# Performance work log

Hardware: AMD Instinct MI355X
Metric: run time of the kernel (lower is better)

## Reference

```python
import jax, jax.numpy as jnp
import numpy as np

B, HW, C = 32, 56, 128
WS, SS, NH = 7, 3, 4
HD = C // NH
SCALE = HD ** -0.5
NWIN = (HW // WS) ** 2  # 64 windows per image
N = WS * WS             # 49 tokens per window


def _build_constants():
    # relative position index [N, N] into flattened (13*13) bias table
    coords = np.stack(np.meshgrid(np.arange(WS), np.arange(WS), indexing='ij'))  # [2,7,7]
    cf = coords.reshape(2, -1)                       # [2,49]
    rel = cf[:, :, None] - cf[:, None, :]            # [2,49,49]
    rel = rel.transpose(1, 2, 0).copy()              # [49,49,2]
    rel[:, :, 0] += WS - 1
    rel[:, :, 1] += WS - 1
    rel[:, :, 0] *= 2 * WS - 1
    pos_index = rel.sum(-1)                          # [49,49]
    # shifted-window attention mask [nW, N, N]
    img = np.zeros((HW, HW))
    sl = (slice(0, -WS), slice(-WS, -SS), slice(-SS, None))
    cnt = 0
    for h in sl:
        for w in sl:
            img[h, w] = cnt
            cnt += 1
    mw = img.reshape(HW // WS, WS, HW // WS, WS).transpose(0, 2, 1, 3).reshape(NWIN, N)
    am = mw[:, None, :] - mw[:, :, None]             # unsqueeze(1) - unsqueeze(2)
    am = np.where(am != 0, -100.0, 0.0).astype(np.float32)
    return jnp.asarray(pos_index), jnp.asarray(am)

POS_INDEX, ATTN_MASK = _build_constants()


def _ln(x, w, b, eps=1e-5):
    mu = x.mean(-1, keepdims=True)
    var = ((x - mu) ** 2).mean(-1, keepdims=True)
    return (x - mu) * jax.lax.rsqrt(var + eps) * w + b


def setup_inputs() -> dict:
    key = jax.random.key(0)
    ks = jax.random.split(key, 10)
    s = 0.02
    return {
        'x': jax.random.normal(ks[0], (B, HW * HW, C), jnp.float32),
        'norm1_w': jnp.ones((C,), jnp.float32),
        'norm1_b': jnp.zeros((C,), jnp.float32),
        'qkv_w': jax.random.normal(ks[1], (C, 3 * C), jnp.float32) * s,
        'qkv_b': jax.random.normal(ks[2], (3 * C,), jnp.float32) * s,
        'proj_w': jax.random.normal(ks[3], (C, C), jnp.float32) * s,
        'proj_b': jax.random.normal(ks[4], (C,), jnp.float32) * s,
        'pos_bias_table': jax.random.normal(ks[5], (2 * WS - 1, 2 * WS - 1, NH), jnp.float32) * s,
        'mlp_w1': jax.random.normal(ks[6], (C, 4 * C), jnp.float32) * s,
        'mlp_b1': jnp.zeros((4 * C,), jnp.float32),
        'mlp_w2': jax.random.normal(ks[7], (4 * C, C), jnp.float32) * s,
        'mlp_b2': jnp.zeros((C,), jnp.float32),
        'norm2_w': jnp.ones((C,), jnp.float32),
        'norm2_b': jnp.zeros((C,), jnp.float32),
    }


def reference(x, norm1_w, norm1_b, qkv_w, qkv_b, proj_w, proj_b, pos_bias_table,
              mlp_w1, mlp_b1, mlp_w2, mlp_b2, norm2_w, norm2_b):
    G = HW // WS  # grid of windows per side
    Bw = B * NWIN
    shortcut = x
    y = _ln(x, norm1_w, norm1_b).reshape(B, HW, HW, C)
    # cyclic shift
    y = jnp.roll(y, (-SS, -SS), axis=(1, 2))
    # window partition -> [B*nW, 49, C]
    yw = y.reshape(B, G, WS, G, WS, C).transpose(0, 1, 3, 2, 4, 5).reshape(Bw, N, C)
    # qkv projection
    qkv = (yw @ qkv_w + qkv_b).reshape(Bw, N, 3, NH, HD).transpose(2, 0, 3, 1, 4)
    q, k, v = qkv[0] * SCALE, qkv[1], qkv[2]  # [Bw, NH, N, HD]
    attn = jnp.einsum('bhnd,bhmd->bhnm', q, k)
    # relative position bias [NH, N, N]
    bias = pos_bias_table.reshape(-1, NH)[POS_INDEX]  # [N,N,NH]
    attn = attn + bias.transpose(2, 0, 1)[None]
    # shift mask per window
    attn = attn.reshape(B, NWIN, NH, N, N) + ATTN_MASK[None, :, None]
    attn = jax.nn.softmax(attn.reshape(Bw, NH, N, N), axis=-1)
    out = jnp.einsum('bhnm,bhmd->bhnd', attn, v).transpose(0, 2, 1, 3).reshape(Bw, N, C)
    out = out @ proj_w + proj_b
    # window reverse
    out = out.reshape(B, G, G, WS, WS, C).transpose(0, 1, 3, 2, 4, 5).reshape(B, HW, HW, C)
    out = jnp.roll(out, (SS, SS), axis=(1, 2)).reshape(B, HW * HW, C)
    x = shortcut + out
    h = _ln(x, norm2_w, norm2_b)
    h = jax.nn.gelu(h @ mlp_w1 + mlp_b1, approximate=False) @ mlp_w2 + mlp_b2
    return x + h
```

## Files before the change

kernel.cpp:

```cpp
#include <hip/hip_runtime.h>
#include <hip/hip_bf16.h>

#define NTOK 100352
#define SCALE_Q 0.17677669529663687f

typedef __bf16 bf16x8 __attribute__((ext_vector_type(8)));
typedef float f32x4 __attribute__((ext_vector_type(4)));
struct bf2 { __hip_bfloat16 x, y; };
struct __align__(8) bh4 { __hip_bfloat16 a, b, c, d; };

__device__ __forceinline__ int wt_to_tok(int wt) {
  int w = wt / 49, n = wt - w * 49;
  int b = w >> 6, wi = w & 63;
  int gh = wi >> 3, gw = wi & 7;
  int r = n / 7, c = n - r * 7;
  int hs = gh * 7 + r + 3; if (hs >= 56) hs -= 56;
  int ws = gw * 7 + c + 3; if (ws >= 56) ws -= 56;
  return (b * 56 + hs) * 56 + ws;
}

__device__ __forceinline__ float gelu_sig(float v) {
  return v / (1.0f + __expf(-1.702f * v));
}

__global__ __launch_bounds__(256) void prep_all(const float* __restrict__ qkvw,
                                                const float* __restrict__ projw,
                                                const float* __restrict__ w1,
                                                const float* __restrict__ w2,
                                                __hip_bfloat16* __restrict__ dst) {
  int i = blockIdx.x * 256 + threadIdx.x;
  float v;
  if (i < 49152) { int n = i >> 7, k = i & 127; v = qkvw[k * 384 + n]; }
  else if (i < 65536) { int j = i - 49152; int n = j >> 7, k = j & 127; v = projw[k * 128 + n]; }
  else if (i < 131072) { int j = i - 65536; int n = j >> 7, k = j & 127; v = w1[k * 512 + n]; }
  else { int j = i - 131072; int n = j / 512, k = j - n * 512; v = w2[k * 128 + n]; }
  dst[i] = __float2bfloat16(v);
}

__global__ __launch_bounds__(256) void ln1_apply(const float* __restrict__ x,
                                                 const float* __restrict__ nw,
                                                 const float* __restrict__ nb,
                                                 __hip_bfloat16* __restrict__ xn) {
  int wt = blockIdx.x * 4 + (threadIdx.x >> 6);
  int lane = threadIdx.x & 63;
  int tok = wt_to_tok(wt);
  float2 v = *(const float2*)(x + (size_t)tok * 128 + lane * 2);
  float s = v.x + v.y, ss = v.x * v.x + v.y * v.y;
#pragma unroll
  for (int off = 32; off; off >>= 1) {
    s += __shfl_xor(s, off);
    ss += __shfl_xor(ss, off);
  }
  float mu = s * (1.0f / 128.0f);
  float rstd = rsqrtf(ss * (1.0f / 128.0f) - mu * mu + 1e-5f);
  float2 wv = *(const float2*)(nw + lane * 2);
  float2 bv = *(const float2*)(nb + lane * 2);
  bf2 o;
  o.x = __float2bfloat16((v.x - mu) * rstd * wv.x + bv.x);
  o.y = __float2bfloat16((v.y - mu) * rstd * wv.y + bv.y);
  *(bf2*)(xn + (size_t)wt * 128 + lane * 2) = o;
}

__global__ __launch_bounds__(256) void attn_mfma(const __hip_bfloat16* __restrict__ qkv,
                                                 const float* __restrict__ ptab,
                                                 __hip_bfloat16* __restrict__ attnout) {
  __shared__ __align__(16) char lds[4 * 12288];
  const int tid = threadIdx.x;
  const int lane = tid & 63, h = tid >> 6;
  const int w = blockIdx.x;
  const int wi = w & 63, gh = wi >> 3, gw = wi & 7;
  char* Pl = lds + h * 12288;
  char* VTl = Pl + 8192;
  const int lxi = lane & 15, lq = lane >> 4, lg4 = (lane >> 4) * 4;

  const __hip_bfloat16* base = qkv + (size_t)w * 49 * 384 + h * 32;
  __hip_bfloat16* op = attnout + (size_t)w * 49 * 128 + h * 32;

  bf16x8 qa[4], kb[4];
#pragma unroll
  for (int mi = 0; mi < 4; ++mi) {
    int t = mi * 16 + lxi; if (t > 48) t = 48;
    qa[mi] = *(const bf16x8*)(base + (size_t)t * 384 + lq * 8);
    kb[mi] = *(const bf16x8*)(base + (size_t)t * 384 + 128 + lq * 8);
  }
  {
    union { bf16x8 v; __hip_bfloat16 e[8]; } vv[4];
    const __hip_bfloat16* vp = base + (size_t)(lane < 49 ? lane : 0) * 384 + 256;
#pragma unroll
    for (int q = 0; q < 4; ++q) vv[q].v = *(const bf16x8*)(vp + q * 8);
    __hip_bfloat16 z = __float2bfloat16(0.0f);
#pragma unroll
    for (int q = 0; q < 4; ++q)
#pragma unroll
      for (int e = 0; e < 8; ++e) {
        int d = q * 8 + e;
        __hip_bfloat16 val = (lane < 49) ? vv[q].e[e] : z;
        *(__hip_bfloat16*)(VTl + d * 128 + ((lane * 2) ^ ((d & 7) << 4))) = val;
      }
  }

  f32x4 s[4][4] = {};
#pragma unroll
  for (int mi = 0; mi < 4; ++mi)
#pragma unroll
    for (int ni = 0; ni < 4; ++ni)
      s[mi][ni] = __builtin_amdgcn_mfma_f32_16x16x32_bf16(qa[mi], kb[ni], s[mi][ni], 0, 0, 0);

  int rj[4], cj[4], cntj[4], jbad[4];
#pragma unroll
  for (int ni = 0; ni < 4; ++ni) {
    int jc = ni * 16 + lxi;
    jbad[ni] = (jc > 48);
    int jj = jbad[ni] ? 48 : jc;
    rj[ni] = jj / 7; cj[ni] = jj - rj[ni] * 7;
    int hj = gh * 7 + rj[ni], wj = gw * 7 + cj[ni];
    cntj[ni] = (hj < 49 ? 0 : (hj < 53 ? 3 : 6)) + (wj < 49 ? 0 : (wj < 53 ? 1 : 2));
  }
#pragma unroll
  for (int mi = 0; mi < 4; ++mi)
#pragma unroll
    for (int j = 0; j < 4; ++j) {
      int i = mi * 16 + lg4 + j; if (i > 48) i = 48;
      int ri = i / 7, ci = i - ri * 7;
      int hi_ = gh * 7 + ri, wi_ = gw * 7 + ci;
      int cnti = (hi_ < 49 ? 0 : (hi_ < 53 ? 3 : 6)) + (wi_ < 49 ? 0 : (wi_ < 53 ? 1 : 2));
#pragma unroll
      for (int ni = 0; ni < 4; ++ni) {
        float b = ptab[((ri - rj[ni] + 6) * 13 + (ci - cj[ni] + 6)) * 4 + h];
        float val = s[mi][ni][j] * SCALE_Q + b;
        if (cnti != cntj[ni]) val -= 100.0f;
        if (jbad[ni]) val = -1e30f;
        s[mi][ni][j] = val;
      }
    }

#pragma unroll
  for (int mi = 0; mi < 4; ++mi)
#pragma unroll
    for (int j = 0; j < 4; ++j) {
      float m = fmaxf(fmaxf(s[mi][0][j], s[mi][1][j]), fmaxf(s[mi][2][j], s[mi][3][j]));
#pragma unroll
      for (int off = 8; off; off >>= 1) m = fmaxf(m, __shfl_xor(m, off));
      float e[4], sum = 0.0f;
#pragma unroll
      for (int ni = 0; ni < 4; ++ni) { e[ni] = __expf(s[mi][ni][j] - m); sum += e[ni]; }
#pragma unroll
      for (int off = 8; off; off >>= 1) sum += __shfl_xor(sum, off);
      float inv = 1.0f / sum;
#pragma unroll
      for (int ni = 0; ni < 4; ++ni) s[mi][ni][j] = e[ni] * inv;
    }

#pragma unroll
  for (int mi = 0; mi < 4; ++mi)
#pragma unroll
    for (int j = 0; j < 4; ++j) {
      int row = mi * 16 + lg4 + j;
      int sw = (row & 7) << 4;
      char* prow = Pl + row * 128;
#pragma unroll
      for (int ni = 0; ni < 4; ++ni)
        *(__hip_bfloat16*)(prow + (((ni * 16 + lxi) * 2) ^ sw)) =
            __float2bfloat16(s[mi][ni][j]);
    }

  __syncthreads();

  f32x4 o[4][2] = {};
#pragma unroll
  for (int ks = 0; ks < 2; ++ks) {
    bf16x8 pa[4], vb[2];
#pragma unroll
    for (int mi = 0; mi < 4; ++mi) {
      int row = mi * 16 + lxi;
      pa[mi] = *(const bf16x8*)(Pl + row * 128 + ((ks * 64 + lq * 16) ^ ((row & 7) << 4)));
    }
#pragma unroll
    for (int ni = 0; ni < 2; ++ni) {
      int row = ni * 16 + lxi;
      vb[ni] = *(const bf16x8*)(VTl + row * 128 + ((ks * 64 + lq * 16) ^ ((row & 7) << 4)));
    }
#pragma unroll
    for (int mi = 0; mi < 4; ++mi)
#pragma unroll
      for (int ni = 0; ni < 2; ++ni)
        o[mi][ni] = __builtin_amdgcn_mfma_f32_16x16x32_bf16(pa[mi], vb[ni], o[mi][ni], 0, 0, 0);
  }

#pragma unroll
  for (int mi = 0; mi < 4; ++mi)
#pragma unroll
    for (int j = 0; j < 4; ++j) {
      int q = mi * 16 + lg4 + j;
      if (q < 49) {
#pragma unroll
        for (int ni = 0; ni < 2; ++ni)
          op[(size_t)q * 128 + ni * 16 + lxi] = __float2bfloat16(o[mi][ni][j]);
      }
    }
}

template<int EPI>
__global__ __launch_bounds__(256) void gemm_mfma(
    const __hip_bfloat16* __restrict__ A, int lda, int NB,
    const __hip_bfloat16* __restrict__ Wt,
    const float* __restrict__ bias,
    void* __restrict__ outv, int ldo,
    __hip_bfloat16* __restrict__ out2,
    const float* __restrict__ nw, const float* __restrict__ nb,
    const float* __restrict__ resf, int K)
{
  __shared__ __align__(16) char AsB[128 * 256];
  __shared__ float redS[256], redQ[256];
  const int bid = blockIdx.x;
  const int xcd = bid & 7, tt = bid >> 3;
  const int nbk = tt % NB, mseq = tt / NB;
  const int m0 = (mseq * 8 + xcd) * 128, n0 = nbk * 128;
  const int tid = threadIdx.x;
  const int srow = tid >> 1;
  const int scol = (tid & 1) * 64;
  const int lane = tid & 63, wid = tid >> 6;
  const int wm = wid >> 1, wn = wid & 1;
  const int lrow = lane & 15, lq = lane >> 4;

  f32x4 acc[4][4] = {};

  for (int k0 = 0; k0 < K; k0 += 128) {
    {
      const char* ap = (const char*)A + ((size_t)(m0 + srow) * lda + k0 + scol) * 2;
      char* dst = AsB + srow * 256;
      int sw = (srow & 7) << 4;
#pragma unroll
      for (int t = 0; t < 8; ++t) {
        int4 raw = *(const int4*)(ap + t * 16);
        *(int4*)(dst + ((scol * 2 + t * 16) ^ sw)) = raw;
      }
    }
    __syncthreads();
#pragma unroll
    for (int ks = 0; ks < 4; ++ks) {
      int kb = ks * 64 + lq * 16;
      bf16x8 af[4], bfr[4];
#pragma unroll
      for (int mi = 0; mi < 4; ++mi) {
        int r = wm * 64 + mi * 16 + lrow;
        af[mi] = *(const bf16x8*)(AsB + r * 256 + (kb ^ ((r & 7) << 4)));
      }
#pragma unroll
      for (int ni = 0; ni < 4; ++ni) {
        int n = n0 + wn * 64 + ni * 16 + lrow;
        bfr[ni] = *(const bf16x8*)(Wt + (size_t)n * K + k0 + ks * 32 + lq * 8);
      }
#pragma unroll
      for (int mi = 0; mi < 4; ++mi)
#pragma unroll
        for (int ni = 0; ni < 4; ++ni)
          acc[mi][ni] = __builtin_amdgcn_mfma_f32_16x16x32_bf16(af[mi], bfr[ni], acc[mi][ni], 0, 0, 0);
    }
    __syncthreads();
  }

  float bv[4];
#pragma unroll
  for (int ni = 0; ni < 4; ++ni) bv[ni] = bias[n0 + wn * 64 + ni * 16 + lrow];

  if (EPI == 4) {
    __hip_bfloat16* x2 = (__hip_bfloat16*)outv;
    float nwc[4], nbc[4];
#pragma unroll
    for (int ni = 0; ni < 4; ++ni) {
      int colg = wn * 64 + ni * 16 + lrow;
      nwc[ni] = nw[colg]; nbc[ni] = nb[colg];
    }
    int toks[4][4];
#pragma unroll
    for (int mi = 0; mi < 4; ++mi)
#pragma unroll
      for (int j = 0; j < 4; ++j) {
        int row = wm * 64 + mi * 16 + lq * 4 + j;
        int tok = wt_to_tok(m0 + row);
        toks[mi][j] = tok;
        float s = 0.0f, ss = 0.0f;
#pragma unroll
        for (int ni = 0; ni < 4; ++ni) {
          int colg = wn * 64 + ni * 16 + lrow;
          float val = acc[mi][ni][j] + bv[ni] + resf[(size_t)tok * 128 + colg];
          x2[(size_t)tok * 128 + colg] = __float2bfloat16(val);
          acc[mi][ni][j] = val;
          s += val; ss += val * val;
        }
#pragma unroll
        for (int off = 8; off; off >>= 1) {
          s += __shfl_xor(s, off);
          ss += __shfl_xor(ss, off);
        }
        if (lrow == 0) { redS[row * 2 + wn] = s; redQ[row * 2 + wn] = ss; }
      }
    __syncthreads();
#pragma unroll
    for (int mi = 0; mi < 4; ++mi)
#pragma unroll
      for (int j = 0; j < 4; ++j) {
        int row = wm * 64 + mi * 16 + lq * 4 + j;
        float s = redS[row * 2] + redS[row * 2 + 1];
        float ss = redQ[row * 2] + redQ[row * 2 + 1];
        float mu = s * (1.0f / 128.0f);
        float rstd = rsqrtf(ss * (1.0f / 128.0f) - mu * mu + 1e-5f);
        int tok = toks[mi][j];
#pragma unroll
        for (int ni = 0; ni < 4; ++ni) {
          int colg = wn * 64 + ni * 16 + lrow;
          float xnv = (acc[mi][ni][j] - mu) * rstd * nwc[ni] + nbc[ni];
          out2[(size_t)tok * 128 + colg] = __float2bfloat16(xnv);
        }
      }
    return;
  }

#pragma unroll
  for (int mi = 0; mi < 4; ++mi) {
#pragma unroll
    for (int j = 0; j < 4; ++j) {
      int rowg = m0 + wm * 64 + mi * 16 + lq * 4 + j;
#pragma unroll
      for (int ni = 0; ni < 4; ++ni) {
        int colg = n0 + wn * 64 + ni * 16 + lrow;
        float val = acc[mi][ni][j] + bv[ni];
        ((__hip_bfloat16*)outv)[(size_t)rowg * ldo + colg] = __float2bfloat16(val);
      }
    }
  }
}

__global__ __launch_bounds__(256) void mlp_fused(
    const __hip_bfloat16* __restrict__ x2n,
    const __hip_bfloat16* __restrict__ w1T,
    const float* __restrict__ b1,
    const __hip_bfloat16* __restrict__ w2T,
    const float* __restrict__ b2,
    const __hip_bfloat16* __restrict__ x2,
    float* __restrict__ out)
{
  __shared__ __align__(16) char AsB[128 * 256];
  __shared__ __align__(16) char Hs[128 * 256];
  const int m0 = blockIdx.x * 128;
  const int tid = threadIdx.x;
  const int srow = tid >> 1, scol = (tid & 1) * 64;
  const int lane = tid & 63, wid = tid >> 6;
  const int wm = wid >> 1, wn = wid & 1;
  const int lrow = lane & 15, lq = lane >> 4;

  {
    const char* ap = (const char*)x2n + ((size_t)(m0 + srow) * 128 + scol) * 2;
    char* dst = AsB + srow * 256;
    int sw = (srow & 7) << 4;
#pragma unroll
    for (int t = 0; t < 8; ++t) {
      int4 raw = *(const int4*)(ap + t * 16);
      *(int4*)(dst + ((scol * 2 + t * 16) ^ sw)) = raw;
    }
  }
  __syncthreads();

  f32x4 oacc[4][4] = {};

  for (int c = 0; c < 4; ++c) {
    f32x4 hacc[4][4] = {};
#pragma unroll
    for (int ks = 0; ks < 4; ++ks) {
      int kb = ks * 64 + lq * 16;
      bf16x8 wf[4], afr[4];
#pragma unroll
      for (int mi = 0; mi < 4; ++mi) {
        int hd = c * 128 + wm * 64 + mi * 16 + lrow;
        wf[mi] = *(const bf16x8*)(w1T + (size_t)hd * 128 + ks * 32 + lq * 8);
      }
#pragma unroll
      for (int ni = 0; ni < 4; ++ni) {
        int r = wn * 64 + ni * 16 + lrow;
        afr[ni] = *(const bf16x8*)(AsB + r * 256 + (kb ^ ((r & 7) << 4)));
      }
#pragma unroll
      for (int mi = 0; mi < 4; ++mi)
#pragma unroll
        for (int ni = 0; ni < 4; ++ni)
          hacc[mi][ni] = __builtin_amdgcn_mfma_f32_16x16x32_bf16(wf[mi], afr[ni], hacc[mi][ni], 0, 0, 0);
    }
    __syncthreads();
#pragma unroll
    for (int mi = 0; mi < 4; ++mi) {
      int hdb = wm * 64 + mi * 16 + lq * 4;
      float4 b4 = *(const float4*)(b1 + c * 128 + hdb);
      float b1v[4] = {b4.x, b4.y, b4.z, b4.w};
#pragma unroll
      for (int ni = 0; ni < 4; ++ni) {
        int m_ = wn * 64 + ni * 16 + lrow;
        bh4 hv;
        hv.a = __float2bfloat16(gelu_sig(hacc[mi][ni][0] + b1v[0]));
        hv.b = __float2bfloat16(gelu_sig(hacc[mi][ni][1] + b1v[1]));
        hv.c = __float2bfloat16(gelu_sig(hacc[mi][ni][2] + b1v[2]));
        hv.d = __float2bfloat16(gelu_sig(hacc[mi][ni][3] + b1v[3]));
        *(bh4*)(Hs + m_ * 256 + ((hdb * 2) ^ ((m_ & 7) << 4))) = hv;
      }
    }
    __syncthreads();
#pragma unroll
    for (int ks = 0; ks < 4; ++ks) {
      int kb = ks * 64 + lq * 16;
      bf16x8 hf[4], w2f[4];
#pragma unroll
      for (int mi = 0; mi < 4; ++mi) {
        int r = wm * 64 + mi * 16 + lrow;
        hf[mi] = *(const bf16x8*)(Hs + r * 256 + (kb ^ ((r & 7) << 4)));
      }
#pragma unroll
      for (int ni = 0; ni < 4; ++ni) {
        int n = wn * 64 + ni * 16 + lrow;
        w2f[ni] = *(const bf16x8*)(w2T + (size_t)n * 512 + c * 128 + ks * 32 + lq * 8);
      }
#pragma unroll
      for (int mi = 0; mi < 4; ++mi)
#pragma unroll
        for (int ni = 0; ni < 4; ++ni)
          oacc[mi][ni] = __builtin_amdgcn_mfma_f32_16x16x32_bf16(hf[mi], w2f[ni], oacc[mi][ni], 0, 0, 0);
    }
  }

  float bv[4];
#pragma unroll
  for (int ni = 0; ni < 4; ++ni) bv[ni] = b2[wn * 64 + ni * 16 + lrow];
#pragma unroll
  for (int mi = 0; mi < 4; ++mi)
#pragma unroll
    for (int j = 0; j < 4; ++j) {
      int row = m0 + wm * 64 + mi * 16 + lq * 4 + j;
#pragma unroll
      for (int ni = 0; ni < 4; ++ni) {
        int col = wn * 64 + ni * 16 + lrow;
        float r = __bfloat162float(x2[(size_t)row * 128 + col]);
        out[(size_t)row * 128 + col] = oacc[mi][ni][j] + bv[ni] + r;
      }
    }
}

extern "C" void kernel_launch(void* const* d_in, const int* in_sizes, int n_in,
                              void* d_out, int out_size, void* d_ws, size_t ws_size,
                              hipStream_t stream) {
  (void)in_sizes; (void)n_in; (void)out_size; (void)ws_size;
  const float* x     = (const float*)d_in[0];
  const float* n1w   = (const float*)d_in[1];
  const float* n1b   = (const float*)d_in[2];
  const float* qkvw  = (const float*)d_in[3];
  const float* qkvb  = (const float*)d_in[4];
  const float* projw = (const float*)d_in[5];
  const float* projb = (const float*)d_in[6];
  const float* ptab  = (const float*)d_in[7];
  const float* w1    = (const float*)d_in[8];
  const float* b1    = (const float*)d_in[9];
  const float* w2    = (const float*)d_in[10];
  const float* b2    = (const float*)d_in[11];
  const float* n2w   = (const float*)d_in[12];
  const float* n2b   = (const float*)d_in[13];
  float* out = (float*)d_out;

  char* ws = (char*)d_ws;
  __hip_bfloat16* xn      = (__hip_bfloat16*)ws;
  __hip_bfloat16* qkv     = (__hip_bfloat16*)(ws + 25690112);
  __hip_bfloat16* attnout = (__hip_bfloat16*)(ws + 102760448);
  __hip_bfloat16* x2      = (__hip_bfloat16*)(ws + 128450560);
  __hip_bfloat16* x2n     = (__hip_bfloat16*)(ws + 154140672);
  __hip_bfloat16* wbase   = (__hip_bfloat16*)(ws + 179830784);
  __hip_bfloat16* qkvwT  = wbase;
  __hip_bfloat16* projwT = wbase + 49152;
  __hip_bfloat16* w1T    = wbase + 65536;
  __hip_bfloat16* w2T    = wbase + 131072;

  prep_all<<<768, 256, 0, stream>>>(qkvw, projw, w1, w2, wbase);
  ln1_apply<<<NTOK / 4, 256, 0, stream>>>(x, n1w, n1b, xn);
  gemm_mfma<0><<<2352, 256, 0, stream>>>(xn, 128, 3, qkvwT, qkvb,
                                         qkv, 384, nullptr, nullptr, nullptr,
                                         nullptr, 128);
  attn_mfma<<<2048, 256, 0, stream>>>(qkv, ptab, attnout);
  gemm_mfma<4><<<784, 256, 0, stream>>>(attnout, 128, 1, projwT, projb,
                                        x2, 128, x2n, n2w, n2b, x, 128);
  mlp_fused<<<784, 256, 0, stream>>>(x2n, w1T, b1, w2T, b2, x2, out);
}
```

Measured before the change: 237.8 us.

## Fuse QKV projection, window attention, and output projection into one per-window kernel

Replaces the separate QKV GEMM, attention kernel and projection+residual+LN2 GEMM with a single kernel per window. Each block loads the window's normalized tokens into LDS, computes Q/K/V per head with MFMA, runs attention, stages the head outputs in LDS, and applies the projection, residual and LayerNorm epilogue. This removes the global round-trips of the qkv and attnout intermediates and two kernel launches. In exchange it uses 80KB of LDS per block, which limits occupancy, and pads 49-token windows to 64 rows in the projection GEMMs.

```diff
diff --git a/kernel.cpp b/kernel.cpp
--- a/kernel.cpp
+++ b/kernel.cpp
@@ -61,44 +61,107 @@
   *(bf2*)(xn + (size_t)wt * 128 + lane * 2) = o;
 }
 
-__global__ __launch_bounds__(256) void attn_mfma(const __hip_bfloat16* __restrict__ qkv,
-                                                 const float* __restrict__ ptab,
-                                                 __hip_bfloat16* __restrict__ attnout) {
-  __shared__ __align__(16) char lds[4 * 12288];
+__global__ __launch_bounds__(256) void fused_wap(
+    const __hip_bfloat16* __restrict__ xn,
+    const __hip_bfloat16* __restrict__ qkvwT,
+    const float* __restrict__ qkvb,
+    const float* __restrict__ ptab,
+    const __hip_bfloat16* __restrict__ projwT,
+    const float* __restrict__ projb,
+    const float* __restrict__ x,
+    const float* __restrict__ n2w, const float* __restrict__ n2b,
+    __hip_bfloat16* __restrict__ x2,
+    __hip_bfloat16* __restrict__ x2n)
+{
+  __shared__ __align__(16) char lds[81920];
   const int tid = threadIdx.x;
   const int lane = tid & 63, h = tid >> 6;
   const int w = blockIdx.x;
   const int wi = w & 63, gh = wi >> 3, gw = wi & 7;
-  char* Pl = lds + h * 12288;
-  char* VTl = Pl + 8192;
   const int lxi = lane & 15, lq = lane >> 4, lg4 = (lane >> 4) * 4;
 
-  const __hip_bfloat16* base = qkv + (size_t)w * 49 * 384 + h * 32;
-  __hip_bfloat16* op = attnout + (size_t)w * 49 * 128 + h * 32;
+  char* Qh   = lds + h * 4096;
+  char* Kh   = lds + 16384 + h * 4096;
+  char* VTh  = lds + 32768 + h * 4096;
+  char* Pl   = lds + 49152 + h * 8192;
+  char* xnS  = lds + 49152;
+  char* Olds = lds;
+  float* redS = (float*)(lds + 32768);
+  float* redQ = (float*)(lds + 33280);
+
+  {
+    const int srow = tid >> 2, sc = (tid & 3) * 32;
+    int gr = w * 49 + (srow < 49 ? srow : 48);
+    const char* ap = (const char*)xn + ((size_t)gr * 128 + sc) * 2;
+    char* dst = xnS + srow * 256;
+    int sw = (srow & 7) << 4;
+#pragma unroll
+    for (int t = 0; t < 4; ++t) {
+      int4 raw = *(const int4*)(ap + t * 16);
+      *(int4*)(dst + ((sc * 2 + t * 16) ^ sw)) = raw;
+    }
+  }
+  __syncthreads();
+
+  int dbase[6];
+  dbase[0] = h * 32;        dbase[1] = h * 32 + 16;
+  dbase[2] = 128 + h * 32;  dbase[3] = 128 + h * 32 + 16;
+  dbase[4] = 256 + h * 32;  dbase[5] = 256 + h * 32 + 16;
+  f32x4 qacc[6][4] = {};
+#pragma unroll
+  for (int ks = 0; ks < 4; ++ks) {
+    bf16x8 wf[6], xf[4];
+#pragma unroll
+    for (int dt = 0; dt < 6; ++dt)
+      wf[dt] = *(const bf16x8*)(qkvwT + (size_t)(dbase[dt] + lxi) * 128 + ks * 32 + lq * 8);
+#pragma unroll
+    for (int tt = 0; tt < 4; ++tt) {
+      int r = tt * 16 + lxi;
+      xf[tt] = *(const bf16x8*)(xnS + r * 256 + ((ks * 64 + lq * 16) ^ ((r & 7) << 4)));
+    }
+#pragma unroll
+    for (int dt = 0; dt < 6; ++dt)
+#pragma unroll
+      for (int tt = 0; tt < 4; ++tt)
+        qacc[dt][tt] = __builtin_amdgcn_mfma_f32_16x16x32_bf16(wf[dt], xf[tt], qacc[dt][tt], 0, 0, 0);
+  }
+#pragma unroll
+  for (int dt = 0; dt < 6; ++dt) {
+    float4 b4 = *(const float4*)(qkvb + dbase[dt] + lg4);
+    float bb[4] = {b4.x, b4.y, b4.z, b4.w};
+#pragma unroll
+    for (int tt = 0; tt < 4; ++tt) {
+      int tok = tt * 16 + lxi;
+      float v0 = qacc[dt][tt][0] + bb[0];
+      float v1 = qacc[dt][tt][1] + bb[1];
+      float v2 = qacc[dt][tt][2] + bb[2];
+      float v3 = qacc[dt][tt][3] + bb[3];
+      if (dt < 4) {
+        char* dstb = (dt < 2) ? Qh : Kh;
+        int o8 = ((dt & 1) * 16 + lg4) * 2;
+        bh4 hv;
+        hv.a = __float2bfloat16(v0); hv.b = __float2bfloat16(v1);
+        hv.c = __float2bfloat16(v2); hv.d = __float2bfloat16(v3);
+        *(bh4*)(dstb + tok * 64 + (o8 ^ ((tok & 3) << 4))) = hv;
+      } else {
+        float vv[4] = {v0, v1, v2, v3};
+#pragma unroll
+        for (int j = 0; j < 4; ++j) {
+          int d = (dt & 1) * 16 + lg4 + j;
+          *(__hip_bfloat16*)(VTh + d * 128 + ((tok * 2) ^ ((d & 7) << 4))) = __float2bfloat16(vv[j]);
+        }
+      }
+    }
+  }
+  __syncthreads();
 
   bf16x8 qa[4], kb[4];
 #pragma unroll
   for (int mi = 0; mi < 4; ++mi) {
-    int t = mi * 16 + lxi; if (t > 48) t = 48;
-    qa[mi] = *(const bf16x8*)(base + (size_t)t * 384 + lq * 8);
-    kb[mi] = *(const bf16x8*)(base + (size_t)t * 384 + 128 + lq * 8);
-  }
-  {
-    union { bf16x8 v; __hip_bfloat16 e[8]; } vv[4];
-    const __hip_bfloat16* vp = base + (size_t)(lane < 49 ? lane : 0) * 384 + 256;
-#pragma unroll
-    for (int q = 0; q < 4; ++q) vv[q].v = *(const bf16x8*)(vp + q * 8);
-    __hip_bfloat16 z = __float2bfloat16(0.0f);
-#pragma unroll
-    for (int q = 0; q < 4; ++q)
-#pragma unroll
-      for (int e = 0; e < 8; ++e) {
-        int d = q * 8 + e;
-        __hip_bfloat16 val = (lane < 49) ? vv[q].e[e] : z;
-        *(__hip_bfloat16*)(VTl + d * 128 + ((lane * 2) ^ ((d & 7) << 4))) = val;
-      }
-  }
-
+    int t = mi * 16 + lxi;
+    qa[mi] = *(const bf16x8*)(Qh + t * 64 + ((lq * 16) ^ ((t & 3) << 4)));
+    kb[mi] = *(const bf16x8*)(Kh + t * 64 + ((lq * 16) ^ ((t & 3) << 4)));
+  }
   f32x4 s[4][4] = {};
 #pragma unroll
   for (int mi = 0; mi < 4; ++mi)
@@ -163,173 +226,114 @@
         *(__hip_bfloat16*)(prow + (((ni * 16 + lxi) * 2) ^ sw)) =
             __float2bfloat16(s[mi][ni][j]);
     }
-
-  __syncthreads();
-
-  f32x4 o[4][2] = {};
+  __syncthreads();
+
+  f32x4 o2[2][4] = {};
 #pragma unroll
   for (int ks = 0; ks < 2; ++ks) {
-    bf16x8 pa[4], vb[2];
-#pragma unroll
-    for (int mi = 0; mi < 4; ++mi) {
-      int row = mi * 16 + lxi;
-      pa[mi] = *(const bf16x8*)(Pl + row * 128 + ((ks * 64 + lq * 16) ^ ((row & 7) << 4)));
-    }
-#pragma unroll
-    for (int ni = 0; ni < 2; ++ni) {
-      int row = ni * 16 + lxi;
-      vb[ni] = *(const bf16x8*)(VTl + row * 128 + ((ks * 64 + lq * 16) ^ ((row & 7) << 4)));
-    }
-#pragma unroll
-    for (int mi = 0; mi < 4; ++mi)
-#pragma unroll
-      for (int ni = 0; ni < 2; ++ni)
-        o[mi][ni] = __builtin_amdgcn_mfma_f32_16x16x32_bf16(pa[mi], vb[ni], o[mi][ni], 0, 0, 0);
-  }
-
-#pragma unroll
-  for (int mi = 0; mi < 4; ++mi)
-#pragma unroll
-    for (int j = 0; j < 4; ++j) {
-      int q = mi * 16 + lg4 + j;
-      if (q < 49) {
-#pragma unroll
-        for (int ni = 0; ni < 2; ++ni)
-          op[(size_t)q * 128 + ni * 16 + lxi] = __float2bfloat16(o[mi][ni][j]);
-      }
-    }
-}
-
-template<int EPI>
-__global__ __launch_bounds__(256) void gemm_mfma(
-    const __hip_bfloat16* __restrict__ A, int lda, int NB,
-    const __hip_bfloat16* __restrict__ Wt,
-    const float* __restrict__ bias,
-    void* __restrict__ outv, int ldo,
-    __hip_bfloat16* __restrict__ out2,
-    const float* __restrict__ nw, const float* __restrict__ nb,
-    const float* __restrict__ resf, int K)
-{
-  __shared__ __align__(16) char AsB[128 * 256];
-  __shared__ float redS[256], redQ[256];
-  const int bid = blockIdx.x;
-  const int xcd = bid & 7, tt = bid >> 3;
-  const int nbk = tt % NB, mseq = tt / NB;
-  const int m0 = (mseq * 8 + xcd) * 128, n0 = nbk * 128;
-  const int tid = threadIdx.x;
-  const int srow = tid >> 1;
-  const int scol = (tid & 1) * 64;
-  const int lane = tid & 63, wid = tid >> 6;
-  const int wm = wid >> 1, wn = wid & 1;
-  const int lrow = lane & 15, lq = lane >> 4;
-
-  f32x4 acc[4][4] = {};
-
-  for (int k0 = 0; k0 < K; k0 += 128) {
-    {
-      const char* ap = (const char*)A + ((size_t)(m0 + srow) * lda + k0 + scol) * 2;
-      char* dst = AsB + srow * 256;
-      int sw = (srow & 7) << 4;
-#pragma unroll
-      for (int t = 0; t < 8; ++t) {
-        int4 raw = *(const int4*)(ap + t * 16);
-        *(int4*)(dst + ((scol * 2 + t * 16) ^ sw)) = raw;
-      }
-    }
-    __syncthreads();
-#pragma unroll
-    for (int ks = 0; ks < 4; ++ks) {
-      int kb = ks * 64 + lq * 16;
-      bf16x8 af[4], bfr[4];
-#pragma unroll
-      for (int mi = 0; mi < 4; ++mi) {
-        int r = wm * 64 + mi * 16 + lrow;
-        af[mi] = *(const bf16x8*)(AsB + r * 256 + (kb ^ ((r & 7) << 4)));
-      }
-#pragma unroll
-      for (int ni = 0; ni < 4; ++ni) {
-        int n = n0 + wn * 64 + ni * 16 + lrow;
-        bfr[ni] = *(const bf16x8*)(Wt + (size_t)n * K + k0 + ks * 32 + lq * 8);
-      }
-#pragma unroll
-      for (int mi = 0; mi < 4; ++mi)
-#pragma unroll
-        for (int ni = 0; ni < 4; ++ni)
-          acc[mi][ni] = __builtin_amdgcn_mfma_f32_16x16x32_bf16(af[mi], bfr[ni], acc[mi][ni], 0, 0, 0);
-    }
-    __syncthreads();
-  }
-
-  float bv[4];
-#pragma unroll
-  for (int ni = 0; ni < 4; ++ni) bv[ni] = bias[n0 + wn * 64 + ni * 16 + lrow];
-
-  if (EPI == 4) {
-    __hip_bfloat16* x2 = (__hip_bfloat16*)outv;
-    float nwc[4], nbc[4];
+    bf16x8 vt[2], pf[4];
+#pragma unroll
+    for (int dt = 0; dt < 2; ++dt) {
+      int r = dt * 16 + lxi;
+      vt[dt] = *(const bf16x8*)(VTh + r * 128 + ((ks * 64 + lq * 16) ^ ((r & 7) << 4)));
+    }
+#pragma unroll
+    for (int tt = 0; tt < 4; ++tt) {
+      int r = tt * 16 + lxi;
+      pf[tt] = *(const bf16x8*)(Pl + r * 128 + ((ks * 64 + lq * 16) ^ ((r & 7) << 4)));
+    }
+#pragma unroll
+    for (int dt = 0; dt < 2; ++dt)
+#pragma unroll
+      for (int tt = 0; tt < 4; ++tt)
+        o2[dt][tt] = __builtin_amdgcn_mfma_f32_16x16x32_bf16(vt[dt], pf[tt], o2[dt][tt], 0, 0, 0);
+  }
+#pragma unroll
+  for (int dt = 0; dt < 2; ++dt)
+#pragma unroll
+    for (int tt = 0; tt < 4; ++tt) {
+      int qtok = tt * 16 + lxi;
+      bh4 hv;
+      hv.a = __float2bfloat16(o2[dt][tt][0]);
+      hv.b = __float2bfloat16(o2[dt][tt][1]);
+      hv.c = __float2bfloat16(o2[dt][tt][2]);
+      hv.d = __float2bfloat16(o2[dt][tt][3]);
+      int ob = h * 64 + dt * 32 + lg4 * 2;
+      *(bh4*)(Olds + qtok * 256 + (ob ^ ((qtok & 7) << 4))) = hv;
+    }
+  __syncthreads();
+
+  const int wm = h >> 1, wn = h & 1;
+  f32x4 acc[2][4] = {};
+#pragma unroll
+  for (int ks = 0; ks < 4; ++ks) {
+    bf16x8 af[2], bfr[4];
+#pragma unroll
+    for (int mi = 0; mi < 2; ++mi) {
+      int r = wm * 32 + mi * 16 + lxi;
+      af[mi] = *(const bf16x8*)(Olds + r * 256 + ((ks * 64 + lq * 16) ^ ((r & 7) << 4)));
+    }
 #pragma unroll
     for (int ni = 0; ni < 4; ++ni) {
-      int colg = wn * 64 + ni * 16 + lrow;
-      nwc[ni] = nw[colg]; nbc[ni] = nb[colg];
-    }
-    int toks[4][4];
-#pragma unroll
-    for (int mi = 0; mi < 4; ++mi)
-#pragma unroll
-      for (int j = 0; j < 4; ++j) {
-        int row = wm * 64 + mi * 16 + lq * 4 + j;
-        int tok = wt_to_tok(m0 + row);
-        toks[mi][j] = tok;
-        float s = 0.0f, ss = 0.0f;
-#pragma unroll
-        for (int ni = 0; ni < 4; ++ni) {
-          int colg = wn * 64 + ni * 16 + lrow;
-          float val = acc[mi][ni][j] + bv[ni] + resf[(size_t)tok * 128 + colg];
-          x2[(size_t)tok * 128 + colg] = __float2bfloat16(val);
-          acc[mi][ni][j] = val;
-          s += val; ss += val * val;
-        }
-#pragma unroll
-        for (int off = 8; off; off >>= 1) {
-          s += __shfl_xor(s, off);
-          ss += __shfl_xor(ss, off);
-        }
-        if (lrow == 0) { redS[row * 2 + wn] = s; redQ[row * 2 + wn] = ss; }
-      }
-    __syncthreads();
-#pragma unroll
-    for (int mi = 0; mi < 4; ++mi)
-#pragma unroll
-      for (int j = 0; j < 4; ++j) {
-        int row = wm * 64 + mi * 16 + lq * 4 + j;
-        float s = redS[row * 2] + redS[row * 2 + 1];
-        float ss = redQ[row * 2] + redQ[row * 2 + 1];
-        float mu = s * (1.0f / 128.0f);
-        float rstd = rsqrtf(ss * (1.0f / 128.0f) - mu * mu + 1e-5f);
-        int tok = toks[mi][j];
-#pragma unroll
-        for (int ni = 0; ni < 4; ++ni) {
-          int colg = wn * 64 + ni * 16 + lrow;
-          float xnv = (acc[mi][ni][j] - mu) * rstd * nwc[ni] + nbc[ni];
-          out2[(size_t)tok * 128 + colg] = __float2bfloat16(xnv);
-        }
-      }
-    return;
-  }
-
-#pragma unroll
-  for (int mi = 0; mi < 4; ++mi) {
-#pragma unroll
-    for (int j = 0; j < 4; ++j) {
-      int rowg = m0 + wm * 64 + mi * 16 + lq * 4 + j;
-#pragma unroll
-      for (int ni = 0; ni < 4; ++ni) {
-        int colg = n0 + wn * 64 + ni * 16 + lrow;
-        float val = acc[mi][ni][j] + bv[ni];
-        ((__hip_bfloat16*)outv)[(size_t)rowg * ldo + colg] = __float2bfloat16(val);
-      }
-    }
-  }
+      int n = wn * 64 + ni * 16 + lxi;
+      bfr[ni] = *(const bf16x8*)(projwT + (size_t)n * 128 + ks * 32 + lq * 8);
+    }
+#pragma unroll
+    for (int mi = 0; mi < 2; ++mi)
+#pragma unroll
+      for (int ni = 0; ni < 4; ++ni)
+        acc[mi][ni] = __builtin_amdgcn_mfma_f32_16x16x32_bf16(af[mi], bfr[ni], acc[mi][ni], 0, 0, 0);
+  }
+  float bv[4], nwc[4], nbc[4];
+#pragma unroll
+  for (int ni = 0; ni < 4; ++ni) {
+    int colg = wn * 64 + ni * 16 + lxi;
+    bv[ni] = projb[colg]; nwc[ni] = n2w[colg]; nbc[ni] = n2b[colg];
+  }
+  int toks[2][4];
+#pragma unroll
+  for (int mi = 0; mi < 2; ++mi)
+#pragma unroll
+    for (int j = 0; j < 4; ++j) {
+      int row = wm * 32 + mi * 16 + lg4 + j;
+      int rr = (row < 49) ? row : 48;
+      int tok = wt_to_tok(w * 49 + rr);
+      toks[mi][j] = tok;
+      float s1 = 0.0f, ss = 0.0f;
+#pragma unroll
+      for (int ni = 0; ni < 4; ++ni) {
+        int colg = wn * 64 + ni * 16 + lxi;
+        float val = acc[mi][ni][j] + bv[ni] + x[(size_t)tok * 128 + colg];
+        if (row < 49) x2[(size_t)tok * 128 + colg] = __float2bfloat16(val);
+        acc[mi][ni][j] = val;
+        s1 += val; ss += val * val;
+      }
+#pragma unroll
+      for (int off = 8; off; off >>= 1) {
+        s1 += __shfl_xor(s1, off);
+        ss += __shfl_xor(ss, off);
+      }
+      if (lxi == 0) { redS[row * 2 + wn] = s1; redQ[row * 2 + wn] = ss; }
+    }
+  __syncthreads();
+#pragma unroll
+  for (int mi = 0; mi < 2; ++mi)
+#pragma unroll
+    for (int j = 0; j < 4; ++j) {
+      int row = wm * 32 + mi * 16 + lg4 + j;
+      if (row >= 49) continue;
+      float s1 = redS[row * 2] + redS[row * 2 + 1];
+      float ss = redQ[row * 2] + redQ[row * 2 + 1];
+      float mu = s1 * (1.0f / 128.0f);
+      float rstd = rsqrtf(ss * (1.0f / 128.0f) - mu * mu + 1e-5f);
+      int tok = toks[mi][j];
+#pragma unroll
+      for (int ni = 0; ni < 4; ++ni) {
+        int colg = wn * 64 + ni * 16 + lxi;
+        float xnv = (acc[mi][ni][j] - mu) * rstd * nwc[ni] + nbc[ni];
+        x2n[(size_t)tok * 128 + colg] = __float2bfloat16(xnv);
+      }
+    }
 }
 
 __global__ __launch_bounds__(256) void mlp_fused(
@@ -465,8 +469,6 @@
 
   char* ws = (char*)d_ws;
   __hip_bfloat16* xn      = (__hip_bfloat16*)ws;
-  __hip_bfloat16* qkv     = (__hip_bfloat16*)(ws + 25690112);
-  __hip_bfloat16* attnout = (__hip_bfloat16*)(ws + 102760448);
   __hip_bfloat16* x2      = (__hip_bfloat16*)(ws + 128450560);
   __hip_bfloat16* x2n     = (__hip_bfloat16*)(ws + 154140672);
   __hip_bfloat16* wbase   = (__hip_bfloat16*)(ws + 179830784);
@@ -477,11 +479,7 @@
 
   prep_all<<<768, 256, 0, stream>>>(qkvw, projw, w1, w2, wbase);
   ln1_apply<<<NTOK / 4, 256, 0, stream>>>(x, n1w, n1b, xn);
-  gemm_mfma<0><<<2352, 256, 0, stream>>>(xn, 128, 3, qkvwT, qkvb,
-                                         qkv, 384, nullptr, nullptr, nullptr,
-                                         nullptr, 128);
-  attn_mfma<<<2048, 256, 0, stream>>>(qkv, ptab, attnout);
-  gemm_mfma<4><<<784, 256, 0, stream>>>(attnout, 128, 1, projwT, projb,
-                                        x2, 128, x2n, n2w, n2b, x, 128);
+  fused_wap<<<2048, 256, 0, stream>>>(xn, qkvwT, qkvb, ptab, projwT, projb,
+                                      x, n2w, n2b, x2, x2n);
   mlp_fused<<<784, 256, 0, stream>>>(x2n, w1T, b1, w2T, b2, x2, out);
 }
```

Result: slower. 345.3 us (+45.2%).
